# Kernel optimization log

Hardware: AMD Instinct MI355X
Metric: run time of the kernel (lower is better)

The kernel has to match this reference:

```python
import jax, jax.numpy as jnp
import numpy as np

B, H, N, D = 64, 12, 196, 768  # ViT-B/16 @ 224: 196 patch tokens + 1 CLS


def setup_inputs() -> dict:
    key = jax.random.key(0)
    k1, k2, k3 = jax.random.split(key, 3)
    student_tokens = jax.random.normal(k1, (B, N, D), dtype=jnp.float32)
    teacher_tokens = jax.random.normal(k2, (B, N, D), dtype=jnp.float32)
    teacher_attn = jax.random.uniform(k3, (B, H, N + 1, N + 1), dtype=jnp.float32)
    return {
        "student_tokens": student_tokens,
        "teacher_tokens": teacher_tokens,
        "teacher_attn": teacher_attn,
    }


def reference(student_tokens, teacher_tokens, teacher_attn):
    s = student_tokens.astype(jnp.float32)
    t = teacher_tokens.astype(jnp.float32)
    # CLS->patch attention, averaged over heads: [B, N]
    w = teacher_attn[:, :, 0, 1:].mean(axis=1)
    w = w / (w.sum(axis=-1, keepdims=True) + 1e-8)
    s = w[..., None] * s
    t = w[..., None] * t
    # center over token dim
    s_c = s - s.mean(axis=1, keepdims=True)
    t_c = t - t.mean(axis=1, keepdims=True)
    tr_s = jnp.sum(s_c * s_c, axis=(1, 2))  # [B]
    tr_t = jnp.sum(t_c * t_c, axis=(1, 2))  # [B]
    # cross-covariance: [B, D, D]
    cross = jnp.einsum("bnd,bne->bde", s_c, t_c)
    # nuclear norm = sum of singular values
    nuclear = jnp.linalg.svd(cross, compute_uv=False).sum(axis=-1)  # [B]
    loss = jnp.maximum(tr_s + tr_t - 2.0 * nuclear, 0.0).mean()
    return loss
```

## Files before the change

### kernel.cpp

```cpp
#include <hip/hip_runtime.h>
#include <hip/hip_bf16.h>
#include <math.h>

#define NTOK 196
#define NDIM 768
#define NB 64
#define NH 12
#define NA 197
#define MAT (NTOK * NTOK)
#define ATTN_HW (NA * NA)
#define POLAR_ITERS 15

#define PADC 208
#define NTILE 13
#define POLAR_LDS_BYTES (2 * NTOK * PADC * 2)

#define GCH 64
#define GPLANE (208 * GCH)
#define GRAM_LDS_BYTES (2 * GPLANE * 2)

#define PTLD 208
#define TRI_WORDS 19306
#define CHOL2_PT_WORDS (16 * PTLD)
#define CHOL2_TRI_OFF CHOL2_PT_WORDS
#define CHOL2_ROWOFF_OFF (CHOL2_TRI_OFF + TRI_WORDS)
#define CHOL2_PV_OFF 22832
#define CHOL2_LDS_BYTES ((CHOL2_PV_OFF + 32) * 4)

typedef __attribute__((ext_vector_type(8))) short short8;
typedef __attribute__((ext_vector_type(4))) short short4_t;
typedef __attribute__((ext_vector_type(4))) float f32x4;

__device__ inline short8 s8zero() { short8 z = {0,0,0,0,0,0,0,0}; return z; }

__device__ inline short f2bf(float f) {
  union { float f; unsigned u; } v; v.f = f;
  unsigned u = v.u;
  u += 0x7fffu + ((u >> 16) & 1u);
  return (short)(u >> 16);
}
__device__ inline float bf2f(short s) {
  union { unsigned u; float f; } v;
  v.u = ((unsigned)(unsigned short)s) << 16;
  return v.f;
}

__global__ void k_w(const float* __restrict__ attn, float* __restrict__ wbuf) {
  int b = blockIdx.x;
  int tid = threadIdx.x;
  __shared__ float red[256];
  float w0 = 0.f;
  if (tid < NTOK) {
    size_t base = (size_t)b * NH * ATTN_HW + 1 + tid;
    #pragma unroll
    for (int h = 0; h < NH; ++h) w0 += attn[base + (size_t)h * ATTN_HW];
    w0 *= (1.f / NH);
  }
  red[tid] = (tid < NTOK) ? w0 : 0.f;
  __syncthreads();
  for (int s = 128; s > 0; s >>= 1) { if (tid < s) red[tid] += red[tid + s]; __syncthreads(); }
  float S = red[0];
  if (tid < NTOK) wbuf[b * NTOK + tid] = w0 / (S + 1e-8f);
}

__global__ __launch_bounds__(512, 1) void k_gram_mfma(
    const float* __restrict__ s, const float* __restrict__ t,
    const float* __restrict__ wbuf, float* __restrict__ Gbuf) {
  extern __shared__ short gsm[];
  short* bhp = gsm;
  short* blp = gsm + GPLANE;
  __shared__ float wsh[NTOK];
  int slot = blockIdx.x, b = slot >> 1, src = slot & 1;
  const float* X = (src ? t : s) + (size_t)b * NTOK * NDIM;
  int tid = threadIdx.x;
  int wave = tid >> 6, ln15 = tid & 15, quad = (tid >> 4) & 3;

  if (tid < NTOK) wsh[tid] = wbuf[b * NTOK + tid];
  for (int i = tid; i < 768; i += 512) {
    int p = i / 384, o = i - p * 384;
    ((int*)(gsm + p * GPLANE + 196 * GCH))[o] = 0;
  }
  __syncthreads();

  f32x4 zz = {0.f, 0.f, 0.f, 0.f};
  f32x4 acc[12];
  #pragma unroll
  for (int j = 0; j < 12; ++j) acc[j] = zz;

  for (int c = 0; c < NDIM / GCH; ++c) {
    int kc = c * GCH;
    for (int gi = tid; gi < NTOK * 8; gi += 512) {
      int r = gi >> 3, g = gi & 7;
      const float* sp = X + (size_t)r * NDIM + kc + g * 8;
      float4 f0 = *(const float4*)(sp);
      float4 f1 = *(const float4*)(sp + 4);
      float wv = wsh[r];
      float vs[8] = {f0.x, f0.y, f0.z, f0.w, f1.x, f1.y, f1.z, f1.w};
      short8 hv, lv;
      #pragma unroll
      for (int e = 0; e < 8; ++e) {
        float y = wv * vs[e];
        short hb = f2bf(y);
        hv[e] = hb;
        lv[e] = f2bf(y - bf2f(hb));
      }
      int pg = (g ^ (r & 7)) * 8;
      *(short8*)(bhp + r * GCH + pg) = hv;
      *(short8*)(blp + r * GCH + pg) = lv;
    }
    __syncthreads();
    #pragma unroll
    for (int j = 0; j < 12; ++j) {
      int T = wave + 8 * j;
      if (T < 91) {
        int ti = (int)((sqrtf(8.f * T + 1.f) - 1.f) * 0.5f);
        if ((ti + 1) * (ti + 2) / 2 <= T) ++ti;
        if (ti * (ti + 1) / 2 > T) --ti;
        int tj = T - ti * (ti + 1) / 2;
        int ra = ti * 16 + ln15, rb = tj * 16 + ln15;
        #pragma unroll
        for (int ks = 0; ks < 2; ++ks) {
          int gb0 = ks * 4 + quad;
          int ga = (gb0 ^ (ra & 7)) * 8, gb = (gb0 ^ (rb & 7)) * 8;
          short8 ah = *(const short8*)(bhp + ra * GCH + ga);
          short8 al = *(const short8*)(blp + ra * GCH + ga);
          short8 bhf = *(const short8*)(bhp + rb * GCH + gb);
          short8 blf = *(const short8*)(blp + rb * GCH + gb);
          acc[j] = __builtin_amdgcn_mfma_f32_16x16x32_bf16(ah, bhf, acc[j], 0, 0, 0);
          acc[j] = __builtin_amdgcn_mfma_f32_16x16x32_bf16(ah, blf, acc[j], 0, 0, 0);
          acc[j] = __builtin_amdgcn_mfma_f32_16x16x32_bf16(al, bhf, acc[j], 0, 0, 0);
        }
      }
    }
    __syncthreads();
  }

  float* G = Gbuf + (size_t)slot * MAT;
  #pragma unroll
  for (int j = 0; j < 12; ++j) {
    int T = wave + 8 * j;
    if (T < 91) {
      int ti = (int)((sqrtf(8.f * T + 1.f) - 1.f) * 0.5f);
      if ((ti + 1) * (ti + 2) / 2 <= T) ++ti;
      if (ti * (ti + 1) / 2 > T) --ti;
      int tj = T - ti * (ti + 1) / 2;
      int col = tj * 16 + ln15;
      #pragma unroll
      for (int r = 0; r < 4; ++r) {
        int row = ti * 16 + quad * 4 + r;
        if (row < NTOK && col < NTOK) {
          G[row * NTOK + col] = acc[j][r];
          if (ti != tj) G[col * NTOK + row] = acc[j][r];
        }
      }
    }
  }
}

__global__ void k_center(float* __restrict__ Gbuf, float* __restrict__ trPb) {
  int slot = blockIdx.x;
  float* A = Gbuf + (size_t)slot * MAT;
  __shared__ float r[NTOK];
  __shared__ float red[256];
  __shared__ float gsh, dsh;
  int tid = threadIdx.x;
  float acc = 0.f;
  if (tid < NTOK) {
    for (int m = 0; m < NTOK; ++m) acc += A[m * NTOK + tid];
    r[tid] = acc * (1.f / NTOK);
  }
  red[tid] = (tid < NTOK) ? acc * (1.f / NTOK) : 0.f;
  __syncthreads();
  for (int s = 128; s > 0; s >>= 1) { if (tid < s) red[tid] += red[tid + s]; __syncthreads(); }
  float g = red[0] * (1.f / NTOK);
  float tv = (tid < NTOK) ? (A[tid * NTOK + tid] - 2.f * r[tid] + g) : 0.f;
  __syncthreads();
  red[tid] = tv;
  __syncthreads();
  for (int s = 128; s > 0; s >>= 1) { if (tid < s) red[tid] += red[tid + s]; __syncthreads(); }
  if (tid == 0) {
    float tr = red[0];
    trPb[slot] = tr;
    gsh = g;
    dsh = 1e-4f * fmaxf(tr, 0.f) * (1.f / NTOK);
  }
  __syncthreads();
  float gg = gsh, dd = dsh;
  for (int idx = tid; idx < MAT; idx += 256) {
    int n = idx / NTOK, m = idx - n * NTOK;
    float v = A[idx] - r[n] - r[m] + gg;
    if (n == m) v += dd;
    A[idx] = v;
  }
}

__global__ __launch_bounds__(256, 1) void k_chol_panel(float* __restrict__ Gbuf) {
  extern __shared__ float smf[];
  float* Pt = smf;
  float* tri = smf + CHOL2_TRI_OFF;
  int* rowoff = (int*)(smf + CHOL2_ROWOFF_OFF);
  float* pvb = smf + CHOL2_PV_OFF;
  int slot = blockIdx.x;
  float* A = Gbuf + (size_t)slot * MAT;
  int tid = threadIdx.x;
  if (tid < NTOK) rowoff[tid] = tid * (tid + 1) / 2;
  __syncthreads();
  for (int idx = tid; idx < MAT; idx += 256) {
    int i = idx / NTOK, j = idx - i * NTOK;
    if (j <= i) tri[rowoff[i] + j] = A[idx];
  }
  __syncthreads();

  for (int k0 = 0; k0 < NTOK; k0 += 16) {
    int nb = (NTOK - k0 < 16) ? (NTOK - k0) : 16;
    int t = tid;
    int i = k0 + t;
    bool hasrow = (t < NTOK - k0);
    int ro = hasrow ? rowoff[i] : 0;

    float a[16];
    #pragma unroll
    for (int jj = 0; jj < 16; ++jj) a[jj] = 0.f;
    if (hasrow) {
      #pragma unroll
      for (int jj = 0; jj < 16; ++jj)
        if (jj < nb && k0 + jj <= i) a[jj] = tri[ro + k0 + jj];
    }

    #pragma unroll
    for (int jj = 0; jj < 16; ++jj) {
      bool cv = (jj < nb);
      if (cv && hasrow && t >= jj && t < nb) pvb[((jj & 1) << 4) + t] = a[jj];
      __syncthreads();
      if (cv && hasrow && t >= jj) {
        const float* pv = pvb + ((jj & 1) << 4);
        f32x4 p0 = *(const f32x4*)(pv);
        f32x4 p1 = *(const f32x4*)(pv + 4);
        f32x4 p2 = *(const f32x4*)(pv + 8);
        f32x4 p3 = *(const f32x4*)(pv + 12);
        float pvj = (jj < 4) ? p0[jj & 3] : (jj < 8) ? p1[jj & 3]
                   : (jj < 12) ? p2[jj & 3] : p3[jj & 3];
        float sq = sqrtf(fmaxf(pvj, 1e-20f));
        float pivinv = 1.f / sq;
        float v = a[jj] * pivinv;
        a[jj] = v;
        #pragma unroll
        for (int m = 0; m < 16; ++m) {
          if (m > jj) {
            float pvm = (m < 4) ? p0[m & 3] : (m < 8) ? p1[m & 3]
                       : (m < 12) ? p2[m & 3] : p3[m & 3];
            if (m < nb) a[m] -= v * (pvm * pivinv);
          }
        }
      }
    }

    if (hasrow) {
      #pragma unroll
      for (int jj = 0; jj < 16; ++jj)
        if (jj < nb && k0 + jj <= i) tri[ro + k0 + jj] = a[jj];
      if (t >= nb) {
        #pragma unroll
        for (int jj = 0; jj < 16; ++jj)
          if (jj < nb) Pt[jj * PTLD + i] = a[jj];
      }
    }
    __syncthreads();

    int k1 = k0 + nb;
    int nrem = NTOK - k1;
    if (nrem > 0) {
      int ntile = (nrem + 3) >> 2;
      int Ttot = ntile * (ntile + 1) / 2;
      for (int T = tid; T < Ttot; T += 256) {
        float disc = (2.f * ntile + 1.f) * (2.f * ntile + 1.f) - 8.f * (float)T;
        int tm = (int)((2.f * ntile + 1.f - sqrtf(fmaxf(disc, 0.f))) * 0.5f);
        if (tm > ntile - 1) tm = ntile - 1;
        if (tm < 0) tm = 0;
        #define FCOL(c) ((c) * ntile - (((c) * ((c) - 1)) >> 1))
        while (tm + 1 <= ntile - 1 && FCOL(tm + 1) <= T) ++tm;
        while (tm > 0 && FCOL(tm) > T) --tm;
        int ti = tm + (T - FCOL(tm));
        #undef FCOL
        int i0 = k1 + ti * 4, m0 = k1 + tm * 4;
        f32x4 acc0 = {0.f, 0.f, 0.f, 0.f};
        f32x4 acc1 = acc0, acc2 = acc0, acc3 = acc0;
        #pragma unroll
        for (int jj = 0; jj < 16; ++jj) {
          if (jj < nb) {
            f32x4 li = *(const f32x4*)(Pt + jj * PTLD + i0);
            f32x4 lm = *(const f32x4*)(Pt + jj * PTLD + m0);
            acc0 += lm * li[0];
            acc1 += lm * li[1];
            acc2 += lm * li[2];
            acc3 += lm * li[3];
          }
        }
        #define STORE_ROW(r, av)                                        \
          { int ii = i0 + (r);                                          \
            if (ii < NTOK) {                                            \
              int roi = rowoff[ii];                                     \
              if (m0 + 0 <= ii) tri[roi + m0 + 0] -= (av)[0];           \
              if (m0 + 1 <= ii) tri[roi + m0 + 1] -= (av)[1];           \
              if (m0 + 2 <= ii) tri[roi + m0 + 2] -= (av)[2];           \
              if (m0 + 3 <= ii) tri[roi + m0 + 3] -= (av)[3];           \
            } }
        STORE_ROW(0, acc0)
        STORE_ROW(1, acc1)
        STORE_ROW(2, acc2)
        STORE_ROW(3, acc3)
        #undef STORE_ROW
      }
    }
    __syncthreads();
  }

  for (int idx = tid; idx < MAT; idx += 256) {
    int i = idx / NTOK, j = idx - i * NTOK;
    A[idx] = (j <= i) ? tri[rowoff[i] + j] : 0.f;
  }
}

__global__ void k_chol_global(float* __restrict__ Gbuf) {
  int slot = blockIdx.x;
  float* A = Gbuf + (size_t)slot * MAT;
  __shared__ float col[NTOK];
  __shared__ float piv;
  int tid = threadIdx.x;
  for (int k = 0; k < NTOK; ++k) {
    if (tid == 0) { float p = sqrtf(fmaxf(A[k * NTOK + k], 1e-20f)); A[k * NTOK + k] = p; piv = p; }
    __syncthreads();
    float inv = 1.f / piv;
    for (int i = k + 1 + tid; i < NTOK; i += 256) {
      float v = A[i * NTOK + k] * inv;
      A[i * NTOK + k] = v;
      col[i] = v;
    }
    for (int j = k + 1 + tid; j < NTOK; j += 256) A[k * NTOK + j] = 0.f;
    __syncthreads();
    int nrem = NTOK - 1 - k;
    int total = nrem * (nrem + 1) / 2;
    for (int tt = tid; tt < total; tt += 256) {
      int a = (int)((sqrtf(8.f * tt + 1.f) - 1.f) * 0.5f);
      while ((a + 1) * (a + 2) / 2 <= tt) ++a;
      while (a * (a + 1) / 2 > tt) --a;
      int bb = tt - a * (a + 1) / 2;
      int i = k + 1 + a, j = k + 1 + bb;
      A[i * NTOK + j] -= col[i] * col[j];
    }
    __syncthreads();
  }
}

__global__ void k_F(const float* __restrict__ Gbuf, float* __restrict__ Fbuf) {
  int b = blockIdx.y;
  const float* Lp = Gbuf + (size_t)(2 * b) * MAT;
  const float* Lq = Gbuf + (size_t)(2 * b + 1) * MAT;
  int ti = blockIdx.x / 7, tj = blockIdx.x % 7;
  int ri = ti * 32, cj = tj * 32;
  __shared__ float As[32][33], Bs[32][33];
  int tid = threadIdx.x, ty = tid >> 4, tx = tid & 15;
  float a00 = 0, a01 = 0, a10 = 0, a11 = 0;
  for (int k0 = 0; k0 < NTOK; k0 += 32) {
    for (int l = tid; l < 1024; l += 256) {
      int kk = l >> 5, ii = l & 31;
      int krow = k0 + kk;
      As[kk][ii] = (krow < NTOK && ri + ii < NTOK) ? Lp[(size_t)krow * NTOK + ri + ii] : 0.f;
      Bs[kk][ii] = (krow < NTOK && cj + ii < NTOK) ? Lq[(size_t)krow * NTOK + cj + ii] : 0.f;
    }
    __syncthreads();
    #pragma unroll
    for (int kk = 0; kk < 32; ++kk) {
      float p0 = As[kk][ty], p1 = As[kk][ty + 16];
      float q0 = Bs[kk][tx], q1 = Bs[kk][tx + 16];
      a00 += p0 * q0; a01 += p0 * q1; a10 += p1 * q0; a11 += p1 * q1;
    }
    __syncthreads();
  }
  float* F = Fbuf + (size_t)b * MAT;
  int i0 = ri + ty, i1 = ri + ty + 16, j0 = cj + tx, j1 = cj + tx + 16;
  if (i0 < NTOK && j0 < NTOK) F[i0 * NTOK + j0] = a00;
  if (i0 < NTOK && j1 < NTOK) F[i0 * NTOK + j1] = a01;
  if (i1 < NTOK && j0 < NTOK) F[i1 * NTOK + j0] = a10;
  if (i1 < NTOK && j1 < NTOK) F[i1 * NTOK + j1] = a11;
}

__global__ void k_pow(const float* __restrict__ Fbuf, float* __restrict__ nrmb) {
  int b = blockIdx.x;
  const float* F = Fbuf + (size_t)b * MAT;
  __shared__ float v[NTOK], u[NTOK];
  __shared__ float red[256];
  int tid = threadIdx.x;
  if (tid < NTOK) v[tid] = 1.f;
  __syncthreads();
  float lastsum = 1.f;
  for (int it = 0; it < 6; ++it) {
    float a = 0.f;
    if (tid < NTOK) { for (int j = 0; j < NTOK; ++j) a += F[tid * NTOK + j] * v[j]; }
    __syncthreads();
    if (tid < NTOK) u[tid] = a;
    __syncthreads();
    float a2 = 0.f;
    if (tid < NTOK) { for (int i = 0; i < NTOK; ++i) a2 += F[i * NTOK + tid] * u[i]; }
    red[tid] = (tid < NTOK) ? a2 * a2 : 0.f;
    __syncthreads();
    for (int s = 128; s > 0; s >>= 1) { if (tid < s) red[tid] += red[tid + s]; __syncthreads(); }
    float sum = red[0];
    lastsum = sum;
    float invn = rsqrtf(sum + 1e-30f);
    __syncthreads();
    if (tid < NTOK) v[tid] = a2 * invn;
    __syncthreads();
  }
  if (tid == 0) {
    float sig = sqrtf(sqrtf(lastsum));
    nrmb[b] = 1.f / (1.1f * sig + 1e-30f);
  }
}

__global__ void k_scale(const float* __restrict__ Fbuf, const float* __restrict__ nrmb,
                        float* __restrict__ X) {
  int b = blockIdx.y;
  int idx = blockIdx.x * 256 + threadIdx.x;
  if (idx < MAT) X[(size_t)b * MAT + idx] = Fbuf[(size_t)b * MAT + idx] * nrmb[b];
}

__global__ __launch_bounds__(512, 1) void k_polar_fused(
    const float* __restrict__ Fbuf, const float* __restrict__ nrmb,
    float* __restrict__ Xout) {
  extern __shared__ short sm[];
  short* bufA = sm;
  short* bufB = sm + NTOK * PADC;
  int b = blockIdx.x;
  const float* F = Fbuf + (size_t)b * MAT;
  float* XO = Xout + (size_t)b * MAT;
  int tid = threadIdx.x;
  int wave = tid >> 6, ln15 = tid & 15, quad = (tid >> 4) & 3;
  int rt0 = wave, rt1 = wave + 8;
  bool has2 = (rt1 < NTILE);

  for (int i = tid; i < (2 * NTOK * PADC) / 2; i += 512) ((int*)sm)[i] = 0;
  __syncthreads();
  float invc = nrmb[b];
  for (int idx = tid; idx < MAT; idx += 512) {
    int i = idx / NTOK, j = idx - i * NTOK;
    bufA[i * PADC + j] = f2bf(F[idx] * invc);
  }
  __syncthreads();

  int arow0 = rt0 * 16 + ln15;
  int arow1 = rt1 * 16 + ln15;
  bool av1 = has2 && (arow1 < NTOK);
  int m0a = rt0 * 16 + quad * 4;
  int m1a = rt1 * 16 + quad * 4;

  for (int it = 0; it < POLAR_ITERS; ++it) {
    {
      short8 a0[7], a1[7];
      #pragma unroll
      for (int ks = 0; ks < 7; ++ks) {
        int kk = ks * 32 + quad * 8;
        a0[ks] = (kk < PADC) ? *(const short8*)(bufA + arow0 * PADC + kk) : s8zero();
        a1[ks] = (av1 && kk < PADC) ? *(const short8*)(bufA + arow1 * PADC + kk) : s8zero();
      }
      for (int ct = 0; ct < NTILE; ++ct) {
        int brow = ct * 16 + ln15;
        bool bv = brow < NTOK;
        f32x4 acc0 = {0.f, 0.f, 0.f, 0.f};
        f32x4 acc1 = {0.f, 0.f, 0.f, 0.f};
        #pragma unroll
        for (int ks = 0; ks < 7; ++ks) {
          int kk = ks * 32 + quad * 8;
          short8 bfr = (bv && kk < PADC) ? *(const short8*)(bufA + brow * PADC + kk) : s8zero();
          acc0 = __builtin_amdgcn_mfma_f32_16x16x32_bf16(a0[ks], bfr, acc0, 0, 0, 0);
          if (has2)
            acc1 = __builtin_amdgcn_mfma_f32_16x16x32_bf16(a1[ks], bfr, acc1, 0, 0, 0);
        }
        if (bv) {
          short4_t w0;
          #pragma unroll
          for (int r = 0; r < 4; ++r) {
            float h = -0.5f * acc0[r] + ((m0a + r == brow) ? 1.5f : 0.f);
            w0[r] = f2bf(h);
          }
          *(short4_t*)(bufB + brow * PADC + m0a) = w0;
          if (has2) {
            short4_t w1;
            #pragma unroll
            for (int r = 0; r < 4; ++r) {
              float h = -0.5f * acc1[r] + ((m1a + r == brow) ? 1.5f : 0.f);
              w1[r] = f2bf(h);
            }
            *(short4_t*)(bufB + brow * PADC + m1a) = w1;
          }
        }
      }
    }
    __syncthreads();
    {
      short8 g0[7], g1[7];
      #pragma unroll
      for (int ks = 0; ks < 7; ++ks) {
        int kk = ks * 32 + quad * 8;
        short8 v0 = s8zero(), v1 = s8zero();
        if (kk < PADC) {
          #pragma unroll
          for (int j = 0; j < 8; ++j) {
            v0[j] = bufA[(kk + j) * PADC + arow0];
            if (has2) v1[j] = bufA[(kk + j) * PADC + arow1];
          }
        }
        g0[ks] = v0; g1[ks] = v1;
      }
      __syncthreads();
      for (int ct = 0; ct < NTILE; ++ct) {
        int n = ct * 16 + ln15;
        bool nv = n < NTOK;
        f32x4 acc0 = {0.f, 0.f, 0.f, 0.f};
        f32x4 acc1 = {0.f, 0.f, 0.f, 0.f};
        #pragma unroll
        for (int ks = 0; ks < 7; ++ks) {
          int kk = ks * 32 + quad * 8;
          short8 bfr = (nv && kk < PADC) ? *(const short8*)(bufB + n * PADC + kk) : s8zero();
          acc0 = __builtin_amdgcn_mfma_f32_16x16x32_bf16(g0[ks], bfr, acc0, 0, 0, 0);
          if (has2)
            acc1 = __builtin_amdgcn_mfma_f32_16x16x32_bf16(g1[ks], bfr, acc1, 0, 0, 0);
        }
        if (nv) {
          short4_t w0;
          #pragma unroll
          for (int r = 0; r < 4; ++r) w0[r] = f2bf(acc0[r]);
          *(short4_t*)(bufA + n * PADC + m0a) = w0;
          if (has2) {
            short4_t w1;
            #pragma unroll
            for (int r = 0; r < 4; ++r) w1[r] = f2bf(acc1[r]);
            *(short4_t*)(bufA + n * PADC + m1a) = w1;
          }
        }
      }
    }
    __syncthreads();
  }

  for (int idx = tid; idx < MAT; idx += 512) {
    int i = idx / NTOK, j = idx - i * NTOK;
    XO[idx] = bf2f(bufA[i * PADC + j]);
  }
}

__global__ void k_xtx(const float* __restrict__ Xb, float* __restrict__ Gp) {
  int b = blockIdx.y;
  const float* X = Xb + (size_t)b * MAT;
  int x = blockIdx.x, ti = 0;
  while (x >= ti + 1) { x -= ti + 1; ++ti; }
  int tj = x;
  int ri = ti * 32, cj = tj * 32;
  __shared__ float As[32][33], Bs[32][33];
  int tid = threadIdx.x, ty = tid >> 4, tx = tid & 15;
  float a00 = 0, a01 = 0, a10 = 0, a11 = 0;
  for (int k0 = 0; k0 < NTOK; k0 += 32) {
    for (int l = tid; l < 1024; l += 256) {
      int kk = l >> 5, ii = l & 31;
      int krow = k0 + kk;
      As[kk][ii] = (krow < NTOK && ri + ii < NTOK) ? X[(size_t)krow * NTOK + ri + ii] : 0.f;
      Bs[kk][ii] = (krow < NTOK && cj + ii < NTOK) ? X[(size_t)krow * NTOK + cj + ii] : 0.f;
    }
    __syncthreads();
    #pragma unroll
    for (int kk = 0; kk < 32; ++kk) {
      float p0 = As[kk][ty], p1 = As[kk][ty + 16];
      float q0 = Bs[kk][tx], q1 = Bs[kk][tx + 16];
      a00 += p0 * q0; a01 += p0 * q1; a10 += p1 * q0; a11 += p1 * q1;
    }
    __syncthreads();
  }
  float* G = Gp + (size_t)b * MAT;
  int i0 = ri + ty, i1 = ri + ty + 16, j0 = cj + tx, j1 = cj + tx + 16;
  if (i0 < NTOK && j0 < NTOK) { G[i0 * NTOK + j0] = a00; G[j0 * NTOK + i0] = a00; }
  if (i0 < NTOK && j1 < NTOK) { G[i0 * NTOK + j1] = a01; G[j1 * NTOK + i0] = a01; }
  if (i1 < NTOK && j0 < NTOK) { G[i1 * NTOK + j0] = a10; G[j0 * NTOK + i1] = a10; }
  if (i1 < NTOK && j1 < NTOK) { G[i1 * NTOK + j1] = a11; G[j1 * NTOK + i1] = a11; }
}

__global__ void k_nsup(const float* __restrict__ Xb, const float* __restrict__ Gp,
                       float* __restrict__ Xn) {
  int b = blockIdx.y;
  const float* X = Xb + (size_t)b * MAT;
  const float* G = Gp + (size_t)b * MAT;
  int ti = blockIdx.x / 7, tj = blockIdx.x % 7;
  int ri = ti * 32, cj = tj * 32;
  __shared__ float As[32][33], Bs[32][33];
  int tid = threadIdx.x, ty = tid >> 4, tx = tid & 15;
  float a00 = 0, a01 = 0, a10 = 0, a11 = 0;
  for (int k0 = 0; k0 < NTOK; k0 += 32) {
    for (int l = tid; l < 1024; l += 256) {
      int rr = l >> 5, cc = l & 31;
      As[rr][cc] = (ri + rr < NTOK && k0 + cc < NTOK) ? X[(size_t)(ri + rr) * NTOK + k0 + cc] : 0.f;
      Bs[rr][cc] = (k0 + rr < NTOK && cj + cc < NTOK) ? G[(size_t)(k0 + rr) * NTOK + cj + cc] : 0.f;
    }
    __syncthreads();
    #pragma unroll
    for (int kk = 0; kk < 32; ++kk) {
      float p0 = As[ty][kk], p1 = As[ty + 16][kk];
      float q0 = Bs[kk][tx], q1 = Bs[kk][tx + 16];
      a00 += p0 * q0; a01 += p0 * q1; a10 += p1 * q0; a11 += p1 * q1;
    }
    __syncthreads();
  }
  float* O = Xn + (size_t)b * MAT;
  int i0 = ri + ty, i1 = ri + ty + 16, j0 = cj + tx, j1 = cj + tx + 16;
  if (i0 < NTOK && j0 < NTOK) O[i0 * NTOK + j0] = 1.5f * X[i0 * NTOK + j0] - 0.5f * a00;
  if (i0 < NTOK && j1 < NTOK) O[i0 * NTOK + j1] = 1.5f * X[i0 * NTOK + j1] - 0.5f * a01;
  if (i1 < NTOK && j0 < NTOK) O[i1 * NTOK + j0] = 1.5f * X[i1 * NTOK + j0] - 0.5f * a10;
  if (i1 < NTOK && j1 < NTOK) O[i1 * NTOK + j1] = 1.5f * X[i1 * NTOK + j1] - 0.5f * a11;
}

__global__ void k_nuc(const float* __restrict__ U, const float* __restrict__ Fbuf,
                      float* __restrict__ nucb) {
  int b = blockIdx.x;
  int tid = threadIdx.x;
  const float* Ub = U + (size_t)b * MAT;
  const float* Fb = Fbuf + (size_t)b * MAT;
  float acc = 0.f;
  for (int idx = tid; idx < MAT; idx += 256) acc += Ub[idx] * Fb[idx];
  __shared__ float red[256];
  red[tid] = acc;
  __syncthreads();
  for (int s = 128; s > 0; s >>= 1) { if (tid < s) red[tid] += red[tid + s]; __syncthreads(); }
  if (tid == 0) nucb[b] = red[0];
}

__global__ void k_final(const float* __restrict__ trPb, const float* __restrict__ nucb,
                        float* __restrict__ out) {
  int tid = threadIdx.x;
  float v = fmaxf(trPb[2 * tid] + trPb[2 * tid + 1] - 2.f * nucb[tid], 0.f);
  #pragma unroll
  for (int off = 32; off; off >>= 1) v += __shfl_down(v, off);
  if (tid == 0) out[0] = v * (1.f / 64.f);
}

extern "C" void kernel_launch(void* const* d_in, const int* in_sizes, int n_in,
                              void* d_out, int out_size, void* d_ws, size_t ws_size,
                              hipStream_t stream) {
  (void)in_sizes; (void)n_in; (void)out_size; (void)ws_size;
  const float* s = (const float*)d_in[0];
  const float* t = (const float*)d_in[1];
  const float* attn = (const float*)d_in[2];
  float* out = (float*)d_out;

  float* W = (float*)d_ws;
  float* Gbuf = W;
  float* Fbuf = Gbuf + (size_t)128 * MAT;
  float* Xbuf = Fbuf + (size_t)64 * MAT;
  float* Xnew = Xbuf + (size_t)64 * MAT;
  float* Gpol = Xnew + (size_t)64 * MAT;
  float* wbuf = Gpol + (size_t)64 * MAT;
  float* trPb = wbuf + (size_t)NB * NTOK;
  float* nucb = trPb + 128;
  float* nrmb = nucb + 64;

  k_w<<<NB, 256, 0, stream>>>(attn, wbuf);
  k_gram_mfma<<<128, 512, GRAM_LDS_BYTES, stream>>>(s, t, wbuf, Gbuf);
  k_center<<<128, 256, 0, stream>>>(Gbuf, trPb);

  hipError_t chol_ok = hipFuncSetAttribute(
      reinterpret_cast<const void*>(k_chol_panel),
      hipFuncAttributeMaxDynamicSharedMemorySize, CHOL2_LDS_BYTES);
  if (chol_ok == hipSuccess) {
    k_chol_panel<<<128, 256, CHOL2_LDS_BYTES, stream>>>(Gbuf);
  } else {
    k_chol_global<<<128, 256, 0, stream>>>(Gbuf);
  }

  k_F<<<dim3(49, 64), 256, 0, stream>>>(Gbuf, Fbuf);
  k_pow<<<64, 256, 0, stream>>>(Fbuf, nrmb);

  hipError_t fused_ok = hipFuncSetAttribute(
      reinterpret_cast<const void*>(k_polar_fused),
      hipFuncAttributeMaxDynamicSharedMemorySize, POLAR_LDS_BYTES);

  const float* finalX;
  if (fused_ok == hipSuccess) {
    k_polar_fused<<<NB, 512, POLAR_LDS_BYTES, stream>>>(Fbuf, nrmb, Xbuf);
    k_xtx<<<dim3(28, 64), 256, 0, stream>>>(Xbuf, Gpol);
    k_nsup<<<dim3(49, 64), 256, 0, stream>>>(Xbuf, Gpol, Xnew);
    k_xtx<<<dim3(28, 64), 256, 0, stream>>>(Xnew, Gpol);
    k_nsup<<<dim3(49, 64), 256, 0, stream>>>(Xnew, Gpol, Xbuf);
    finalX = Xbuf;
  } else {
    k_scale<<<dim3(151, 64), 256, 0, stream>>>(Fbuf, nrmb, Xbuf);
    float* Xc = Xbuf;
    float* Xn = Xnew;
    for (int it = 0; it < POLAR_ITERS; ++it) {
      k_xtx<<<dim3(28, 64), 256, 0, stream>>>(Xc, Gpol);
      k_nsup<<<dim3(49, 64), 256, 0, stream>>>(Xc, Gpol, Xn);
      float* tmp = Xc; Xc = Xn; Xn = tmp;
    }
    finalX = Xc;
  }

  k_nuc<<<64, 256, 0, stream>>>(finalX, Fbuf, nucb);
  k_final<<<1, 64, 0, stream>>>(trPb, nucb, out);
}
```

Before: 991.8 us.

## Swizzle polar LDS layout and stage power-iteration matrix in LDS

The fused polar Newton-Schulz kernel now stores its bf16 matrices in LDS with an XOR swizzle on 8-element groups. This is meant to reduce bank conflicts on the row and column (transposed) reads and the short4 writes. A new power-iteration kernel first copies the 196x196 F matrix into padded LDS, so the 6 iterations of matvec and transposed matvec read from shared memory instead of global memory. The cost is about 155KB of LDS per block in the power kernel and extra index arithmetic in the polar kernel's inner loops.

```diff
diff --git a/kernel.cpp b/kernel.cpp
--- a/kernel.cpp
+++ b/kernel.cpp
@@ -19,6 +19,10 @@
 #define GPLANE (208 * GCH)
 #define GRAM_LDS_BYTES (2 * GPLANE * 2)
 
+#define POW_LD 197
+#define POW_F_WORDS (NTOK * POW_LD)
+#define POW_LDS_BYTES ((POW_F_WORDS + 2 * NTOK + 256) * 4)
+
 #define PTLD 208
 #define TRI_WORDS 19306
 #define CHOL2_PT_WORDS (16 * PTLD)
@@ -43,6 +47,12 @@
   union { unsigned u; float f; } v;
   v.u = ((unsigned)(unsigned short)s) << 16;
   return v.f;
+}
+
+__device__ inline int swz_g(int g, int r) {
+  if (g < 16) return g ^ (r & 7);
+  else if (g < 24) return 16 + ((g - 16) ^ (r & 7));
+  else return 24 + ((g - 24) ^ (r & 1));
 }
 
 __global__ void k_w(const float* __restrict__ attn, float* __restrict__ wbuf) {
@@ -385,6 +395,48 @@
   if (i1 < NTOK && j1 < NTOK) F[i1 * NTOK + j1] = a11;
 }
 
+__global__ __launch_bounds__(256, 1) void k_pow_lds(const float* __restrict__ Fbuf,
+                                                    float* __restrict__ nrmb) {
+  extern __shared__ float psm[];
+  float* Fsh = psm;
+  float* v = psm + POW_F_WORDS;
+  float* u = v + NTOK;
+  float* red = u + NTOK;
+  int b = blockIdx.x;
+  const float* F = Fbuf + (size_t)b * MAT;
+  int tid = threadIdx.x;
+  for (int idx = tid; idx < MAT; idx += 256) {
+    int i = idx / NTOK, j = idx - i * NTOK;
+    Fsh[i * POW_LD + j] = F[idx];
+  }
+  if (tid < NTOK) v[tid] = 1.f;
+  __syncthreads();
+  float lastsum = 1.f;
+  for (int it = 0; it < 6; ++it) {
+    if (tid < NTOK) {
+      float a = 0.f;
+      for (int j = 0; j < NTOK; ++j) a += Fsh[tid * POW_LD + j] * v[j];
+      u[tid] = a;
+    }
+    __syncthreads();
+    float a2 = 0.f;
+    if (tid < NTOK) { for (int i = 0; i < NTOK; ++i) a2 += Fsh[i * POW_LD + tid] * u[i]; }
+    red[tid] = (tid < NTOK) ? a2 * a2 : 0.f;
+    __syncthreads();
+    for (int s2 = 128; s2 > 0; s2 >>= 1) { if (tid < s2) red[tid] += red[tid + s2]; __syncthreads(); }
+    float sum = red[0];
+    lastsum = sum;
+    float invn = rsqrtf(sum + 1e-30f);
+    __syncthreads();
+    if (tid < NTOK) v[tid] = a2 * invn;
+    __syncthreads();
+  }
+  if (tid == 0) {
+    float sig = sqrtf(sqrtf(lastsum));
+    nrmb[b] = 1.f / (1.1f * sig + 1e-30f);
+  }
+}
+
 __global__ void k_pow(const float* __restrict__ Fbuf, float* __restrict__ nrmb) {
   int b = blockIdx.x;
   const float* F = Fbuf + (size_t)b * MAT;
@@ -444,7 +496,7 @@
   float invc = nrmb[b];
   for (int idx = tid; idx < MAT; idx += 512) {
     int i = idx / NTOK, j = idx - i * NTOK;
-    bufA[i * PADC + j] = f2bf(F[idx] * invc);
+    bufA[i * PADC + swz_g(j >> 3, i) * 8 + (j & 7)] = f2bf(F[idx] * invc);
   }
   __syncthreads();
 
@@ -453,6 +505,11 @@
   bool av1 = has2 && (arow1 < NTOK);
   int m0a = rt0 * 16 + quad * 4;
   int m1a = rt1 * 16 + quad * 4;
+  int gq0 = 2 * rt0 + (quad >> 1);
+  int gq1 = 2 * rt1 + (quad >> 1);
+  int wsub = (quad & 1) * 4;
+  int ga0 = arow0 >> 3, go0 = arow0 & 7;
+  int ga1 = arow1 >> 3, go1 = arow1 & 7;
 
   for (int it = 0; it < POLAR_ITERS; ++it) {
     {
@@ -460,8 +517,12 @@
       #pragma unroll
       for (int ks = 0; ks < 7; ++ks) {
         int kk = ks * 32 + quad * 8;
-        a0[ks] = (kk < PADC) ? *(const short8*)(bufA + arow0 * PADC + kk) : s8zero();
-        a1[ks] = (av1 && kk < PADC) ? *(const short8*)(bufA + arow1 * PADC + kk) : s8zero();
+        int g = ks * 4 + quad;
+        a0[ks] = (kk < PADC) ? *(const short8*)(bufA + arow0 * PADC + swz_g(g, arow0) * 8)
+                             : s8zero();
+        a1[ks] = (av1 && kk < PADC)
+                     ? *(const short8*)(bufA + arow1 * PADC + swz_g(g, arow1) * 8)
+                     : s8zero();
       }
       for (int ct = 0; ct < NTILE; ++ct) {
         int brow = ct * 16 + ln15;
@@ -471,7 +532,10 @@
         #pragma unroll
         for (int ks = 0; ks < 7; ++ks) {
           int kk = ks * 32 + quad * 8;
-          short8 bfr = (bv && kk < PADC) ? *(const short8*)(bufA + brow * PADC + kk) : s8zero();
+          int g = ks * 4 + quad;
+          short8 bfr = (bv && kk < PADC)
+                           ? *(const short8*)(bufA + brow * PADC + swz_g(g, brow) * 8)
+                           : s8zero();
           acc0 = __builtin_amdgcn_mfma_f32_16x16x32_bf16(a0[ks], bfr, acc0, 0, 0, 0);
           if (has2)
             acc1 = __builtin_amdgcn_mfma_f32_16x16x32_bf16(a1[ks], bfr, acc1, 0, 0, 0);
@@ -483,7 +547,7 @@
             float h = -0.5f * acc0[r] + ((m0a + r == brow) ? 1.5f : 0.f);
             w0[r] = f2bf(h);
           }
-          *(short4_t*)(bufB + brow * PADC + m0a) = w0;
+          *(short4_t*)(bufB + brow * PADC + swz_g(gq0, brow) * 8 + wsub) = w0;
           if (has2) {
             short4_t w1;
             #pragma unroll
@@ -491,7 +555,7 @@
               float h = -0.5f * acc1[r] + ((m1a + r == brow) ? 1.5f : 0.f);
               w1[r] = f2bf(h);
             }
-            *(short4_t*)(bufB + brow * PADC + m1a) = w1;
+            *(short4_t*)(bufB + brow * PADC + swz_g(gq1, brow) * 8 + wsub) = w1;
           }
         }
       }
@@ -506,8 +570,9 @@
         if (kk < PADC) {
           #pragma unroll
           for (int j = 0; j < 8; ++j) {
-            v0[j] = bufA[(kk + j) * PADC + arow0];
-            if (has2) v1[j] = bufA[(kk + j) * PADC + arow1];
+            int rr = kk + j;
+            v0[j] = bufA[rr * PADC + swz_g(ga0, rr) * 8 + go0];
+            if (has2) v1[j] = bufA[rr * PADC + swz_g(ga1, rr) * 8 + go1];
           }
         }
         g0[ks] = v0; g1[ks] = v1;
@@ -521,7 +586,10 @@
         #pragma unroll
         for (int ks = 0; ks < 7; ++ks) {
           int kk = ks * 32 + quad * 8;
-          short8 bfr = (nv && kk < PADC) ? *(const short8*)(bufB + n * PADC + kk) : s8zero();
+          int g = ks * 4 + quad;
+          short8 bfr = (nv && kk < PADC)
+                           ? *(const short8*)(bufB + n * PADC + swz_g(g, n) * 8)
+                           : s8zero();
           acc0 = __builtin_amdgcn_mfma_f32_16x16x32_bf16(g0[ks], bfr, acc0, 0, 0, 0);
           if (has2)
             acc1 = __builtin_amdgcn_mfma_f32_16x16x32_bf16(g1[ks], bfr, acc1, 0, 0, 0);
@@ -530,12 +598,12 @@
           short4_t w0;
           #pragma unroll
           for (int r = 0; r < 4; ++r) w0[r] = f2bf(acc0[r]);
-          *(short4_t*)(bufA + n * PADC + m0a) = w0;
+          *(short4_t*)(bufA + n * PADC + swz_g(gq0, n) * 8 + wsub) = w0;
           if (has2) {
             short4_t w1;
             #pragma unroll
             for (int r = 0; r < 4; ++r) w1[r] = f2bf(acc1[r]);
-            *(short4_t*)(bufA + n * PADC + m1a) = w1;
+            *(short4_t*)(bufA + n * PADC + swz_g(gq1, n) * 8 + wsub) = w1;
           }
         }
       }
@@ -545,7 +613,7 @@
 
   for (int idx = tid; idx < MAT; idx += 512) {
     int i = idx / NTOK, j = idx - i * NTOK;
-    XO[idx] = bf2f(bufA[i * PADC + j]);
+    XO[idx] = bf2f(bufA[i * PADC + swz_g(j >> 3, i) * 8 + (j & 7)]);
   }
 }
 
@@ -674,7 +742,15 @@
   }
 
   k_F<<<dim3(49, 64), 256, 0, stream>>>(Gbuf, Fbuf);
-  k_pow<<<64, 256, 0, stream>>>(Fbuf, nrmb);
+
+  hipError_t pow_ok = hipFuncSetAttribute(
+      reinterpret_cast<const void*>(k_pow_lds),
+      hipFuncAttributeMaxDynamicSharedMemorySize, POW_LDS_BYTES);
+  if (pow_ok == hipSuccess) {
+    k_pow_lds<<<64, 256, POW_LDS_BYTES, stream>>>(Fbuf, nrmb);
+  } else {
+    k_pow<<<64, 256, 0, stream>>>(Fbuf, nrmb);
+  }
 
   hipError_t fused_ok = hipFuncSetAttribute(
       reinterpret_cast<const void*>(k_polar_fused),
```

New measurement: 1.015 ms. 2.4% more time.
